# Performance work log

Measured on AMD Instinct MI355X. Metric: run time of the kernel, lower is better.

The kernel has to match this reference:

```python
import jax, jax.numpy as jnp
import numpy as np

C = 256
CQK = C // 8  # 32

def setup_inputs() -> dict:
    key = jax.random.key(0)
    ks = jax.random.split(key, 8)
    N, L = 8, 4096
    x = jax.random.normal(ks[0], (N, C, L), dtype=jnp.float32)
    s = 1.0 / np.sqrt(C)
    Wq = jax.random.normal(ks[1], (CQK, C), dtype=jnp.float32) * s
    bq = jnp.zeros((CQK,), dtype=jnp.float32)
    Wk = jax.random.normal(ks[2], (CQK, C), dtype=jnp.float32) * s
    bk = jnp.zeros((CQK,), dtype=jnp.float32)
    Wv = jax.random.normal(ks[3], (C, C), dtype=jnp.float32) * s
    bv = jnp.zeros((C,), dtype=jnp.float32)
    gamma = jnp.ones((1,), dtype=jnp.float32) * 0.5  # nonzero so output depends on attention
    return {"x": x, "Wq": Wq, "bq": bq, "Wk": Wk, "bk": bk, "Wv": Wv, "bv": bv, "gamma": gamma}

def reference(x, Wq, bq, Wk, bk, Wv, bv, gamma):
    # conv1d with kernel_size=1 == pointwise linear over channel dim
    q = jnp.einsum('ncl,oc->nol', x, Wq) + bq[None, :, None]   # (N, C/8, L)
    k = jnp.einsum('ncl,oc->nol', x, Wk) + bk[None, :, None]   # (N, C/8, L)
    v = jnp.einsum('ncl,oc->nol', x, Wv) + bv[None, :, None]   # (N, C, L)
    # energy[n, i, j] = q[n, :, i] . k[n, :, j]
    energy = jnp.einsum('nci,ncj->nij', q, k)                  # (N, L, L)
    attention = jax.nn.softmax(energy, axis=-1)
    # out[n, c, i] = sum_j v[n, c, j] * attention[n, i, j]
    out = jnp.einsum('ncj,nij->nci', v, attention)             # (N, C, L)
    return gamma * out + x
```

## Files before the change

### kernel.cpp

```cpp
#include <hip/hip_runtime.h>
#include <hip/hip_bf16.h>

#define NB 8
#define CC 256
#define LL 4096
#define CQ 32

typedef __bf16 bf16x8 __attribute__((ext_vector_type(8)));
typedef float f32x4 __attribute__((ext_vector_type(4)));
typedef unsigned short u16x4 __attribute__((ext_vector_type(4)));

union B8u { bf16x8 b; u16x4 h[2]; };
union P4u { u16x4 u; __bf16 e[4]; };

#define WS_QT  ((size_t)0)
#define WS_KT  ((size_t)1048576)
#define WS_VV  ((size_t)2097152)
#define WS_WQ  ((size_t)18874368)
#define WS_BQ  ((size_t)18882560)
#define WS_WK  ((size_t)18882592)
#define WS_BK  ((size_t)18890784)
#define WS_WV  ((size_t)18890816)
#define WS_BV  ((size_t)18956352)

__device__ __forceinline__ bool tag_is_bf16(const void* gamma_raw) {
  return *(const unsigned short*)gamma_raw != 0;
}
__device__ __forceinline__ float cvt_load(const void* p, size_t i, bool b16) {
  return b16 ? (float)((const __bf16*)p)[i] : ((const float*)p)[i];
}

__global__ __launch_bounds__(256) void convert_wb_kernel(
    const void* __restrict__ Wq, const void* __restrict__ bq,
    const void* __restrict__ Wk, const void* __restrict__ bk,
    const void* __restrict__ Wv, const void* __restrict__ bv,
    const void* __restrict__ gm, __bf16* __restrict__ ws)
{
  const bool b16 = tag_is_bf16(gm);
  int t = blockIdx.x * 256 + threadIdx.x;
  for (int i = t; i < 82240; i += 32 * 256) {
    float v; size_t dof;
    if (i < 8192)       { v = cvt_load(Wq, i, b16);         dof = WS_WQ + i; }
    else if (i < 8224)  { v = cvt_load(bq, i - 8192, b16);  dof = WS_BQ + (i - 8192); }
    else if (i < 16416) { v = cvt_load(Wk, i - 8224, b16);  dof = WS_WK + (i - 8224); }
    else if (i < 16448) { v = cvt_load(bk, i - 16416, b16); dof = WS_BK + (i - 16416); }
    else if (i < 81984) { v = cvt_load(Wv, i - 16448, b16); dof = WS_WV + (i - 16448); }
    else                { v = cvt_load(bv, i - 81984, b16); dof = WS_BV + (i - 81984); }
    ws[dof] = (__bf16)v;
  }
}

__global__ __launch_bounds__(256, 2) void proj_kernel(
    const void* __restrict__ x_raw, const void* __restrict__ gm_raw,
    __bf16* __restrict__ ws)
{
  const bool b16 = tag_is_bf16(gm_raw);
  const int bid = blockIdx.x;
  const int n = bid & 7, l0 = (bid >> 3) * 64;
  const int tid = threadIdx.x;
  const int w = tid >> 6, lane = tid & 63, li = lane & 15, qd = lane >> 4;

  __shared__ __align__(16) __bf16 tmp[64][72];
  __shared__ __align__(16) __bf16 xlt[64][264];

  for (int cb = 0; cb < 4; ++cb) {
    __syncthreads();
    #pragma unroll
    for (int p = 0; p < 2; ++p) {
      int cc = (tid >> 3) + p * 32;
      int lc = (tid & 7) * 8;
      size_t off = (size_t)n * CC * LL + (size_t)(cb * 64 + cc) * LL + l0 + lc;
      bf16x8 val;
      if (b16) {
        val = *(const bf16x8*)((const __bf16*)x_raw + off);
      } else {
        const float* xf = (const float*)x_raw + off;
        f32x4 a = *(const f32x4*)xf;
        f32x4 b = *(const f32x4*)(xf + 4);
        #pragma unroll
        for (int s = 0; s < 4; ++s) { val[s] = (__bf16)a[s]; val[s + 4] = (__bf16)b[s]; }
      }
      *(bf16x8*)(&tmp[cc][lc]) = val;
    }
    __syncthreads();
    #pragma unroll
    for (int p = 0; p < 2; ++p) {
      int lx = (tid >> 3) + p * 32;
      int cw = (tid & 7) * 8;
      bf16x8 o;
      #pragma unroll
      for (int s = 0; s < 8; ++s) o[s] = tmp[cw + s][lx];
      *(bf16x8*)(&xlt[lx][cb * 64 + cw]) = o;
    }
  }
  __syncthreads();

  const __bf16* Wqk = (w < 2) ? (ws + WS_WQ) : (ws + WS_WK);
  const __bf16* Wv  = ws + WS_WV;
  const int obase = (w & 1) * 16;

  f32x4 vacc[4][4];
  f32x4 qkacc[4];
  #pragma unroll
  for (int a = 0; a < 4; ++a) {
    qkacc[a] = f32x4{0, 0, 0, 0};
    #pragma unroll
    for (int b = 0; b < 4; ++b) vacc[a][b] = f32x4{0, 0, 0, 0};
  }

  for (int k0 = 0; k0 < CC; k0 += 32) {
    bf16x8 xf[4];
    #pragma unroll
    for (int lt = 0; lt < 4; ++lt)
      xf[lt] = *(const bf16x8*)(&xlt[lt * 16 + li][k0 + qd * 8]);
    bf16x8 wa = *(const bf16x8*)(Wqk + (size_t)(obase + li) * CC + k0 + qd * 8);
    #pragma unroll
    for (int lt = 0; lt < 4; ++lt)
      qkacc[lt] = __builtin_amdgcn_mfma_f32_16x16x32_bf16(wa, xf[lt], qkacc[lt], 0, 0, 0);
    #pragma unroll
    for (int ct = 0; ct < 4; ++ct) {
      bf16x8 wb = *(const bf16x8*)(Wv + (size_t)(w * 64 + ct * 16 + li) * CC + k0 + qd * 8);
      #pragma unroll
      for (int lt = 0; lt < 4; ++lt)
        vacc[lt][ct] = __builtin_amdgcn_mfma_f32_16x16x32_bf16(xf[lt], wb, vacc[lt][ct], 0, 0, 0);
    }
  }

  {
    const __bf16* bqk = (w < 2) ? (ws + WS_BQ) : (ws + WS_BK);
    __bf16* dqk = ((w < 2) ? (ws + WS_QT) : (ws + WS_KT)) + (size_t)n * LL * CQ;
    float bf[4];
    #pragma unroll
    for (int rr = 0; rr < 4; ++rr) bf[rr] = (float)bqk[obase + qd * 4 + rr];
    #pragma unroll
    for (int lt = 0; lt < 4; ++lt) {
      P4u pk;
      #pragma unroll
      for (int rr = 0; rr < 4; ++rr) pk.e[rr] = (__bf16)(qkacc[lt][rr] + bf[rr]);
      *(u16x4*)(dqk + (size_t)(l0 + lt * 16 + li) * CQ + obase + qd * 4) = pk.u;
    }
  }
  {
    __bf16* dv = ws + WS_VV + (size_t)n * 128 * CC * 32;
    #pragma unroll
    for (int ct = 0; ct < 4; ++ct) {
      int c = w * 64 + ct * 16 + li;
      float bvf = (float)(ws + WS_BV)[c];
      #pragma unroll
      for (int lt = 0; lt < 4; ++lt) {
        int jl = lt * 16 + qd * 4;
        int jb = (l0 + jl) >> 5, jj = jl & 31;
        P4u pk;
        #pragma unroll
        for (int rr = 0; rr < 4; ++rr) pk.e[rr] = (__bf16)(vacc[lt][ct][rr] + bvf);
        *(u16x4*)(dv + ((size_t)jb * CC + c) * 32 + jj) = pk.u;
      }
    }
  }
}

__global__ __launch_bounds__(1024, 4) void attn_kernel(
    const __bf16* __restrict__ ws, const void* __restrict__ x_raw,
    const void* __restrict__ gamma_raw, void* __restrict__ out_raw)
{
  const int bid = blockIdx.x;
  const int n = bid & 7, iblk = (bid >> 3) * 128;
  const int tid = threadIdx.x, w = tid >> 6, lane = tid & 63;
  const int li = lane & 15, qd = lane >> 4;
  const int it = w & 7, jh = w >> 3;
  const int cg = w & 7, jg = w >> 3;

  const __bf16* qtn = ws + WS_QT + (size_t)n * LL * CQ;
  const __bf16* ktn = ws + WS_KT + (size_t)n * LL * CQ;
  const __bf16* v2n = ws + WS_VV + (size_t)n * 128 * CC * 32;

  __shared__ __align__(16) __bf16 plds[2][4][8][16][36];
  __shared__ __align__(16) float  lbuf[16][16];
  __shared__ __align__(16) __bf16 olds[256][72];
  float* scratch = (float*)&plds[0][0][0][0][0];

  bf16x8 qfrag = *(const bf16x8*)(qtn + (size_t)(iblk + it * 16 + li) * CQ + qd * 8);
  const f32x4 zero = {0.f, 0.f, 0.f, 0.f};

  f32x4 oacc[16];
  #pragma unroll
  for (int t = 0; t < 16; ++t) oacc[t] = zero;
  float lp = 0.f;

  bf16x8 kf[4];
  #pragma unroll
  for (int u = 0; u < 4; ++u)
    kf[u] = *(const bf16x8*)(ktn + (size_t)(jh * 64 + u * 16 + li) * CQ + qd * 8);

  for (int js = 0; js < LL; js += 128) {
    const int buf = (js >> 7) & 1;
    bf16x8 vf[4];
    #pragma unroll
    for (int s = 0; s < 2; ++s) {
      const int jb = (js >> 5) + jg * 2 + s;
      #pragma unroll
      for (int ct = 0; ct < 2; ++ct)
        vf[s * 2 + ct] = *(const bf16x8*)(v2n + ((size_t)jb * CC + cg * 32 + ct * 16 + li) * 32 + qd * 8);
    }
    #pragma unroll
    for (int u = 0; u < 4; ++u) {
      f32x4 s = __builtin_amdgcn_mfma_f32_16x16x32_bf16(kf[u], qfrag, zero, 0, 0, 0);
      P4u pk;
      #pragma unroll
      for (int r = 0; r < 4; ++r) {
        float e = __expf(s[r]); lp += e; pk.e[r] = (__bf16)e;
      }
      *(u16x4*)(&plds[buf][jh * 2 + (u >> 1)][it][li][(u & 1) * 16 + qd * 4]) = pk.u;
    }
    {
      const int jn = (js + 128 < LL) ? (js + 128) : 0;
      #pragma unroll
      for (int u = 0; u < 4; ++u)
        kf[u] = *(const bf16x8*)(ktn + (size_t)(jn + jh * 64 + u * 16 + li) * CQ + qd * 8);
    }
    __syncthreads();
    #pragma unroll
    for (int s = 0; s < 2; ++s) {
      #pragma unroll
      for (int tt = 0; tt < 8; ++tt) {
        B8u ap;
        ap.b = *(const bf16x8*)(&plds[buf][jg * 2 + s][tt][li][qd * 8]);
        oacc[tt * 2 + 0] = __builtin_amdgcn_mfma_f32_16x16x32_bf16(ap.b, vf[s * 2 + 0], oacc[tt * 2 + 0], 0, 0, 0);
        oacc[tt * 2 + 1] = __builtin_amdgcn_mfma_f32_16x16x32_bf16(ap.b, vf[s * 2 + 1], oacc[tt * 2 + 1], 0, 0, 0);
      }
    }
  }

  lp += __shfl_xor(lp, 16);
  lp += __shfl_xor(lp, 32);
  lbuf[it * 2 + jh][li] = lp;
  __syncthreads();

  #pragma unroll
  for (int r = 0; r < 2; ++r) {
    if (jg == 1 && (cg >> 2) == r) {
      float* d = scratch + (size_t)(cg & 3) * 4096;
      #pragma unroll
      for (int t = 0; t < 16; ++t)
        *(f32x4*)(d + t * 256 + lane * 4) = oacc[t];
    }
    __syncthreads();
    if (jg == 0 && (cg >> 2) == r) {
      const float* s = scratch + (size_t)(cg & 3) * 4096;
      #pragma unroll
      for (int t = 0; t < 16; ++t)
        oacc[t] += *(const f32x4*)(s + t * 256 + lane * 4);
    }
    __syncthreads();
  }

  const bool b16 = tag_is_bf16(gamma_raw);
  const float gma = b16 ? (float)(*(const __bf16*)gamma_raw)
                        : (*(const float*)gamma_raw);

  f32x4 gi[8];
  if (jg == 0) {
    #pragma unroll
    for (int pp = 0; pp < 8; ++pp) {
      f32x4 l0v = *(const f32x4*)(&lbuf[pp * 2 + 0][qd * 4]);
      f32x4 l1v = *(const f32x4*)(&lbuf[pp * 2 + 1][qd * 4]);
      #pragma unroll
      for (int rr = 0; rr < 4; ++rr) gi[pp][rr] = gma / (l0v[rr] + l1v[rr]);
    }
  }

  const int ec = tid >> 5, i2 = (tid & 31) * 2;
  #pragma unroll
  for (int h = 0; h < 2; ++h) {
    if (jg == 0) {
      #pragma unroll
      for (int pi = 0; pi < 4; ++pi) {
        const int pp = h * 4 + pi;
        #pragma unroll
        for (int ct = 0; ct < 2; ++ct) {
          P4u pk;
          #pragma unroll
          for (int rr = 0; rr < 4; ++rr)
            pk.e[rr] = (__bf16)(oacc[pp * 2 + ct][rr] * gi[pp][rr]);
          *(u16x4*)(&olds[cg * 32 + ct * 16 + li][pi * 16 + qd * 4]) = pk.u;
        }
      }
    }
    __syncthreads();
    const int ibase = iblk + h * 64;
    if (b16) {
      const __bf16* xn = (const __bf16*)x_raw + (size_t)n * CC * LL;
      __bf16* outn = (__bf16*)out_raw + (size_t)n * CC * LL;
      for (int c = ec; c < CC; c += 32) {
        unsigned int ov = *(const unsigned int*)(&olds[c][i2]);
        unsigned int xv = *(const unsigned int*)(xn + (size_t)c * LL + ibase + i2);
        const __bf16* op = (const __bf16*)&ov;
        const __bf16* xp = (const __bf16*)&xv;
        unsigned int res;
        __bf16* rp = (__bf16*)&res;
        rp[0] = (__bf16)((float)op[0] + (float)xp[0]);
        rp[1] = (__bf16)((float)op[1] + (float)xp[1]);
        *(unsigned int*)(outn + (size_t)c * LL + ibase + i2) = res;
      }
    } else {
      const float* xn = (const float*)x_raw + (size_t)n * CC * LL;
      float* outn = (float*)out_raw + (size_t)n * CC * LL;
      for (int c = ec; c < CC; c += 32) {
        unsigned int ov = *(const unsigned int*)(&olds[c][i2]);
        const __bf16* op = (const __bf16*)&ov;
        float2 xv = *(const float2*)(xn + (size_t)c * LL + ibase + i2);
        float2 res;
        res.x = (float)op[0] + xv.x;
        res.y = (float)op[1] + xv.y;
        *(float2*)(outn + (size_t)c * LL + ibase + i2) = res;
      }
    }
    __syncthreads();
  }
}

extern "C" void kernel_launch(void* const* d_in, const int* in_sizes, int n_in,
                              void* d_out, int out_size, void* d_ws, size_t ws_size,
                              hipStream_t stream) {
  (void)in_sizes; (void)n_in; (void)out_size; (void)ws_size;
  __bf16* ws = (__bf16*)d_ws;

  hipLaunchKernelGGL(convert_wb_kernel, dim3(32), dim3(256), 0, stream,
                     d_in[1], d_in[2], d_in[3], d_in[4], d_in[5], d_in[6],
                     d_in[7], ws);
  hipLaunchKernelGGL(proj_kernel, dim3(512), dim3(256), 0, stream,
                     d_in[0], d_in[7], ws);
  hipLaunchKernelGGL(attn_kernel, dim3(256), dim3(1024), 0, stream,
                     (const __bf16*)ws, d_in[0], d_in[7], d_out);
}
```

Baseline: 198.0 us.

## Retile PV stage per wave to 64 channels by 64 rows and split V loads

Changes the per-wave PV tile from 32 channels by 128 query rows to 64 channels by 64 query rows. Each P fragment read from LDS is now reused across four MFMAs instead of two, which halves LDS reads of P. The second V slice is loaded after the barrier so its latency overlaps the MFMAs of the first slice. The __syncthreads is also swapped for a custom lgkmcnt wait plus s_barrier, so outstanding global loads (next K and V) are not drained at the barrier. The epilogue is remapped to match the new tiling. The custom barrier depends on exact waitcnt semantics and adds a little risk.

```diff
diff --git a/kernel.cpp b/kernel.cpp
--- a/kernel.cpp
+++ b/kernel.cpp
@@ -28,6 +28,10 @@
 }
 __device__ __forceinline__ float cvt_load(const void* p, size_t i, bool b16) {
   return b16 ? (float)((const __bf16*)p)[i] : ((const float*)p)[i];
+}
+
+__device__ __forceinline__ void lds_barrier() {
+  asm volatile("s_waitcnt lgkmcnt(0)\n\ts_barrier" ::: "memory");
 }
 
 __global__ __launch_bounds__(256) void convert_wb_kernel(
@@ -168,7 +172,8 @@
   const int tid = threadIdx.x, w = tid >> 6, lane = tid & 63;
   const int li = lane & 15, qd = lane >> 4;
   const int it = w & 7, jh = w >> 3;
-  const int cg = w & 7, jg = w >> 3;
+  const int cs = w & 3, ih = (w >> 2) & 1;
+  const int jg = jh;
 
   const __bf16* qtn = ws + WS_QT + (size_t)n * LL * CQ;
   const __bf16* ktn = ws + WS_KT + (size_t)n * LL * CQ;
@@ -194,13 +199,12 @@
 
   for (int js = 0; js < LL; js += 128) {
     const int buf = (js >> 7) & 1;
-    bf16x8 vf[4];
-    #pragma unroll
-    for (int s = 0; s < 2; ++s) {
-      const int jb = (js >> 5) + jg * 2 + s;
-      #pragma unroll
-      for (int ct = 0; ct < 2; ++ct)
-        vf[s * 2 + ct] = *(const bf16x8*)(v2n + ((size_t)jb * CC + cg * 32 + ct * 16 + li) * 32 + qd * 8);
+    bf16x8 vf0[4];
+    {
+      const int jb = (js >> 5) + jg * 2;
+      #pragma unroll
+      for (int ct = 0; ct < 4; ++ct)
+        vf0[ct] = *(const bf16x8*)(v2n + ((size_t)jb * CC + cs * 64 + ct * 16 + li) * 32 + qd * 8);
     }
     #pragma unroll
     for (int u = 0; u < 4; ++u) {
@@ -218,15 +222,24 @@
       for (int u = 0; u < 4; ++u)
         kf[u] = *(const bf16x8*)(ktn + (size_t)(jn + jh * 64 + u * 16 + li) * CQ + qd * 8);
     }
-    __syncthreads();
+    lds_barrier();
+    bf16x8 vf1[4];
+    {
+      const int jb = (js >> 5) + jg * 2 + 1;
+      #pragma unroll
+      for (int ct = 0; ct < 4; ++ct)
+        vf1[ct] = *(const bf16x8*)(v2n + ((size_t)jb * CC + cs * 64 + ct * 16 + li) * 32 + qd * 8);
+    }
     #pragma unroll
     for (int s = 0; s < 2; ++s) {
       #pragma unroll
-      for (int tt = 0; tt < 8; ++tt) {
+      for (int tt = 0; tt < 4; ++tt) {
         B8u ap;
-        ap.b = *(const bf16x8*)(&plds[buf][jg * 2 + s][tt][li][qd * 8]);
-        oacc[tt * 2 + 0] = __builtin_amdgcn_mfma_f32_16x16x32_bf16(ap.b, vf[s * 2 + 0], oacc[tt * 2 + 0], 0, 0, 0);
-        oacc[tt * 2 + 1] = __builtin_amdgcn_mfma_f32_16x16x32_bf16(ap.b, vf[s * 2 + 1], oacc[tt * 2 + 1], 0, 0, 0);
+        ap.b = *(const bf16x8*)(&plds[buf][jg * 2 + s][ih * 4 + tt][li][qd * 8]);
+        #pragma unroll
+        for (int ct = 0; ct < 4; ++ct)
+          oacc[tt * 4 + ct] = __builtin_amdgcn_mfma_f32_16x16x32_bf16(
+              ap.b, (s ? vf1[ct] : vf0[ct]), oacc[tt * 4 + ct], 0, 0, 0);
       }
     }
   }
@@ -238,15 +251,15 @@
 
   #pragma unroll
   for (int r = 0; r < 2; ++r) {
-    if (jg == 1 && (cg >> 2) == r) {
-      float* d = scratch + (size_t)(cg & 3) * 4096;
+    if (jg == 1 && ih == r) {
+      float* d = scratch + (size_t)cs * 4096;
       #pragma unroll
       for (int t = 0; t < 16; ++t)
         *(f32x4*)(d + t * 256 + lane * 4) = oacc[t];
     }
     __syncthreads();
-    if (jg == 0 && (cg >> 2) == r) {
-      const float* s = scratch + (size_t)(cg & 3) * 4096;
+    if (jg == 0 && ih == r) {
+      const float* s = scratch + (size_t)cs * 4096;
       #pragma unroll
       for (int t = 0; t < 16; ++t)
         oacc[t] += *(const f32x4*)(s + t * 256 + lane * 4);
@@ -258,31 +271,31 @@
   const float gma = b16 ? (float)(*(const __bf16*)gamma_raw)
                         : (*(const float*)gamma_raw);
 
-  f32x4 gi[8];
+  f32x4 gi[4];
   if (jg == 0) {
     #pragma unroll
-    for (int pp = 0; pp < 8; ++pp) {
+    for (int tt = 0; tt < 4; ++tt) {
+      const int pp = ih * 4 + tt;
       f32x4 l0v = *(const f32x4*)(&lbuf[pp * 2 + 0][qd * 4]);
       f32x4 l1v = *(const f32x4*)(&lbuf[pp * 2 + 1][qd * 4]);
       #pragma unroll
-      for (int rr = 0; rr < 4; ++rr) gi[pp][rr] = gma / (l0v[rr] + l1v[rr]);
+      for (int rr = 0; rr < 4; ++rr) gi[tt][rr] = gma / (l0v[rr] + l1v[rr]);
     }
   }
 
   const int ec = tid >> 5, i2 = (tid & 31) * 2;
   #pragma unroll
   for (int h = 0; h < 2; ++h) {
-    if (jg == 0) {
-      #pragma unroll
-      for (int pi = 0; pi < 4; ++pi) {
-        const int pp = h * 4 + pi;
+    if (jg == 0 && ih == h) {
+      #pragma unroll
+      for (int tt = 0; tt < 4; ++tt) {
         #pragma unroll
-        for (int ct = 0; ct < 2; ++ct) {
+        for (int ct = 0; ct < 4; ++ct) {
           P4u pk;
           #pragma unroll
           for (int rr = 0; rr < 4; ++rr)
-            pk.e[rr] = (__bf16)(oacc[pp * 2 + ct][rr] * gi[pp][rr]);
-          *(u16x4*)(&olds[cg * 32 + ct * 16 + li][pi * 16 + qd * 4]) = pk.u;
+            pk.e[rr] = (__bf16)(oacc[tt * 4 + ct][rr] * gi[tt][rr]);
+          *(u16x4*)(&olds[cs * 64 + ct * 16 + li][tt * 16 + qd * 4]) = pk.u;
         }
       }
     }
```

New measurement: 401.7 us. +102.8%, slower.
